# Performance work log

Measured on AMD Instinct MI355X. Metric: run time of the kernel, lower is better.

The kernel has to match this reference:

```python
import jax, jax.numpy as jnp
import numpy as np

N, H, R, E = 100000, 128, 30, 600000
EPS = 1e-5  # BatchNorm1d default eps


def _rgcn_layer(h, src, dst, etype, W, root, bias):
    """PyG RGCNConv: out = h @ root + bias + sum_r scatter_mean_r(h[src] @ W[r]).
    Mean is per (dst, relation) edge count."""
    n = h.shape[0]
    r_count = W.shape[0]
    seg = dst * r_count + etype                      # combined (dst, rel) segment id
    deg = jax.ops.segment_sum(jnp.ones_like(etype, dtype=h.dtype), seg,
                              num_segments=n * r_count)
    norm = 1.0 / jnp.maximum(deg[seg], 1.0)          # (E,) per-edge mean weight

    def body(out, inp):
        Wr, r = inp
        xr = h @ Wr                                  # (N,H) relation-transformed feats
        contrib = jnp.where((etype == r)[:, None], xr[src] * norm[:, None], 0.0)
        return out + jax.ops.segment_sum(contrib, dst, num_segments=n), None

    out0 = h @ root + bias
    out, _ = jax.lax.scan(body, out0, (W, jnp.arange(r_count)))
    return out


def _bn_relu(h, gamma, beta):
    # BatchNorm1d in training mode: biased batch statistics over the node dim
    mu = h.mean(axis=0)
    var = h.var(axis=0)
    return jax.nn.relu((h - mu) * jax.lax.rsqrt(var + EPS) * gamma + beta)


def setup_inputs() -> dict:
    key = jax.random.key(0)
    ks = jax.random.split(key, 16)
    s = 1.0 / np.sqrt(H)
    return {
        "x": jnp.arange(N, dtype=jnp.int32),
        "edge_index": jax.random.randint(ks[0], (2, E), 0, N, dtype=jnp.int32),
        "edge_type": jax.random.randint(ks[1], (E,), 0, R, dtype=jnp.int32),
        "emb": jax.random.normal(ks[2], (N, H), jnp.float32) * s,
        "W1": jax.random.normal(ks[3], (R, H, H), jnp.float32) * s,
        "root1": jax.random.normal(ks[4], (H, H), jnp.float32) * s,
        "b1": jnp.zeros((H,), jnp.float32),
        "g1": jnp.ones((H,), jnp.float32),
        "be1": jnp.zeros((H,), jnp.float32),
        "W2": jax.random.normal(ks[5], (R, H, H), jnp.float32) * s,
        "root2": jax.random.normal(ks[6], (H, H), jnp.float32) * s,
        "b2": jnp.zeros((H,), jnp.float32),
        "g2": jnp.ones((H,), jnp.float32),
        "be2": jnp.zeros((H,), jnp.float32),
    }


def reference(x, edge_index, edge_type, emb, W1, root1, b1, g1, be1,
              W2, root2, b2, g2, be2):
    src, dst = edge_index[0], edge_index[1]
    h = emb[x]                                        # (N,H) embedding lookup
    h = _bn_relu(_rgcn_layer(h, src, dst, edge_type, W1, root1, b1), g1, be1)
    h = _bn_relu(_rgcn_layer(h, src, dst, edge_type, W2, root2, b2), g2, be2)
    return h  # dropout is identity (deterministic reference)
```

## Files before the change

kernel.cpp:

```cpp
#include <hip/hip_runtime.h>
#include <hip/hip_bf16.h>

#define NN 100000
#define HH 128
#define RR 30
#define NE 600000
#define TILE 64
#define CH 64
#define EPAD (NE + RR * TILE)
#define NCHMAX (EPAD / TILE)
#define NB_PS ((NN + 255) / 256)
#define NBLK_BN 784
#define RPB_BN 128
#define BN_EPS 1e-5f

typedef __bf16 v8bf __attribute__((ext_vector_type(8)));
typedef float  v4f  __attribute__((ext_vector_type(4)));

static __device__ __forceinline__ unsigned short f2b(float f) {
    unsigned int u = __float_as_uint(f);
    unsigned int r = (u + 0x7FFF + ((u >> 16) & 1)) >> 16;
    return (unsigned short)r;
}

__global__ void k_hist(const int* __restrict__ dst, const int* __restrict__ et,
                       int* __restrict__ deg, int* __restrict__ cnt) {
    __shared__ int lh[RR];
    int t = threadIdx.x;
    if (t < RR) lh[t] = 0;
    __syncthreads();
    int i = blockIdx.x * blockDim.x + t;
    if (i < NE) {
        int d = dst[i], r = et[i];
        atomicAdd(&deg[d * RR + r], 1);
        atomicAdd(&lh[r], 1);
    }
    __syncthreads();
    if (t < RR && lh[t]) atomicAdd(&cnt[t], lh[t]);
}

__global__ void k_degsum(const int* __restrict__ deg, int* __restrict__ cnt_d) {
    int d = blockIdx.x * blockDim.x + threadIdx.x;
    if (d >= NN) return;
    int s = 0;
#pragma unroll
    for (int r = 0; r < RR; ++r) s += deg[(size_t)d * RR + r];
    cnt_d[d] = s;
}

__global__ void k_scan(const int* __restrict__ cnt, int* __restrict__ cursor,
                       int* __restrict__ totals,
                       int* __restrict__ src_s, int* __restrict__ dst_s,
                       float* __restrict__ norm_s, int* __restrict__ dpos_s,
                       int* __restrict__ chunk_rel, int need_dst) {
    __shared__ int off[RR + 1];
    if (threadIdx.x == 0) {
        int acc = 0;
        for (int r = 0; r < RR; ++r) {
            off[r] = acc;
            acc += (cnt[r] + TILE - 1) / TILE;
        }
        off[RR] = acc;
        totals[0] = acc * TILE;
    }
    __syncthreads();
    for (int r = 0; r < RR; ++r) {
        for (int c = off[r] + (int)threadIdx.x; c < off[r + 1]; c += blockDim.x)
            chunk_rel[c] = r;
        int begin = off[r] * TILE + cnt[r];
        int end   = off[r + 1] * TILE;
        for (int p = begin + (int)threadIdx.x; p < end; p += blockDim.x) {
            src_s[p] = 0; norm_s[p] = 0.f;
            dpos_s[p] = NE;
            if (need_dst) dst_s[p] = 0;
        }
    }
    if (threadIdx.x == 0)
        for (int r = 0; r < RR; ++r) cursor[r] = off[r] * TILE;
}

__global__ void k_psum1(const int* __restrict__ c, int* __restrict__ bsum) {
    __shared__ int sh[256];
    int i = blockIdx.x * 256 + threadIdx.x;
    sh[threadIdx.x] = (i < NN) ? c[i] : 0;
    __syncthreads();
    for (int s = 128; s > 0; s >>= 1) {
        if (threadIdx.x < s) sh[threadIdx.x] += sh[threadIdx.x + s];
        __syncthreads();
    }
    if (threadIdx.x == 0) bsum[blockIdx.x] = sh[0];
}

__global__ void k_psum2(int* __restrict__ bsum) {
    __shared__ int sh[512];
    int t = threadIdx.x;
    sh[t] = (t < NB_PS) ? bsum[t] : 0;
    __syncthreads();
    if (t == 0) {
        int acc = 0;
        for (int b = 0; b < NB_PS; ++b) { int v = sh[b]; sh[b] = acc; acc += v; }
    }
    __syncthreads();
    if (t < NB_PS) bsum[t] = sh[t];
}

__global__ void k_psum3(const int* __restrict__ c, const int* __restrict__ bscan,
                        int* __restrict__ off, int* __restrict__ cur) {
    __shared__ int sh[256];
    int t = threadIdx.x;
    int i = blockIdx.x * 256 + t;
    int v = (i < NN) ? c[i] : 0;
    sh[t] = v;
    __syncthreads();
    for (int s = 1; s < 256; s <<= 1) {
        int a = (t >= s) ? sh[t - s] : 0;
        __syncthreads();
        sh[t] += a;
        __syncthreads();
    }
    int excl = sh[t] - v + bscan[blockIdx.x];
    if (i < NN) { off[i] = excl; cur[i] = excl; }
    if (i == 0) off[NN] = NE;
}

__global__ void k_fillds2(const int* __restrict__ off, int* __restrict__ ds2) {
    int d = blockIdx.x * blockDim.x + threadIdx.x;
    if (d >= NN) return;
    int s = off[d], e = off[d + 1];
    for (int p = s; p < e; ++p) ds2[p] = d;
}

__global__ void k_scatter(const int* __restrict__ src, const int* __restrict__ dst,
                          const int* __restrict__ et, const int* __restrict__ deg,
                          int* __restrict__ cursor, int* __restrict__ cursor_dst,
                          int* __restrict__ src_s, int* __restrict__ dst_s,
                          float* __restrict__ norm_s, int* __restrict__ dpos_s,
                          int need_dst) {
    __shared__ int lh[RR];
    __shared__ int lbase[RR];
    int t = threadIdx.x;
    if (t < RR) lh[t] = 0;
    __syncthreads();
    int i = blockIdx.x * blockDim.x + t;
    int r = 0, d = 0, lrank = 0;
    bool valid = (i < NE);
    if (valid) {
        r = et[i]; d = dst[i];
        lrank = atomicAdd(&lh[r], 1);
    }
    __syncthreads();
    if (t < RR && lh[t]) lbase[t] = atomicAdd(&cursor[t], lh[t]);
    __syncthreads();
    if (valid) {
        int pos = lbase[r] + lrank;
        src_s[pos] = src[i];
        if (need_dst) dst_s[pos] = d;
        int dg = deg[d * RR + r];
        norm_s[pos] = 1.0f / (float)(dg > 1 ? dg : 1);
        dpos_s[pos] = atomicAdd(&cursor_dst[d], 1);
    }
}

__global__ void k_convW(const float* __restrict__ W, unsigned short* __restrict__ Wt,
                        int total) {
    int idx = blockIdx.x * blockDim.x + threadIdx.x;
    if (idx >= total) return;
    int m = idx / (HH * HH);
    int rem = idx % (HH * HH);
    int k = rem / HH, c = rem % HH;
    Wt[m * HH * HH + c * HH + k] = f2b(W[idx]);
}

__global__ void k_embed(const int* __restrict__ x, const float* __restrict__ emb,
                        unsigned short* __restrict__ hb) {
    int idx = blockIdx.x * blockDim.x + threadIdx.x;
    if (idx >= NN * HH) return;
    int i = idx / HH, j = idx % HH;
    hb[idx] = f2b(emb[x[i] * HH + j]);
}

__global__ __launch_bounds__(256) void k_rootgemm(const unsigned short* __restrict__ hb,
                                                  const unsigned short* __restrict__ rootT,
                                                  const float* __restrict__ bias,
                                                  float* __restrict__ tmp) {
    __shared__ __align__(16) unsigned short Xs[TILE][HH + 8];
    __shared__ __align__(16) unsigned short Ws[HH][HH + 8];
    int base = blockIdx.x * TILE;
    int t = threadIdx.x;

    {
        int l = t >> 2, lr = t & 3;
        int row = base + l;
        for (int i = 0; i < 4; ++i) {
            int g = lr + 4 * i;
            uint4 v = {0u, 0u, 0u, 0u};
            if (row < NN) v = *reinterpret_cast<const uint4*>(hb + (size_t)row * HH + g * 8);
            *reinterpret_cast<uint4*>(&Xs[l][g * 8]) = v;
        }
    }
    for (int i = 0; i < 8; ++i) {
        int idx = t + 256 * i;
        int row = idx >> 4, g = idx & 15;
        *reinterpret_cast<uint4*>(&Ws[row][g * 8]) =
            *reinterpret_cast<const uint4*>(rootT + row * HH + g * 8);
    }
    __syncthreads();

    int w = t >> 6, lane = t & 63;
    int lr16 = lane & 15, kg = lane >> 4;
    v4f acc[8];
    for (int n = 0; n < 8; ++n) acc[n] = (v4f){0.f, 0.f, 0.f, 0.f};
#pragma unroll
    for (int kk = 0; kk < 4; ++kk) {
        int k0 = kk * 32 + kg * 8;
        v8bf a = *reinterpret_cast<const v8bf*>(&Xs[w * 16 + lr16][k0]);
#pragma unroll
        for (int n = 0; n < 8; ++n) {
            v8bf b = *reinterpret_cast<const v8bf*>(&Ws[n * 16 + lr16][k0]);
            acc[n] = __builtin_amdgcn_mfma_f32_16x16x32_bf16(a, b, acc[n], 0, 0, 0);
        }
    }
#pragma unroll
    for (int n = 0; n < 8; ++n)
        for (int j = 0; j < 4; ++j) {
            int row = base + w * 16 + kg * 4 + j;
            int col = n * 16 + lr16;
            if (row < NN) tmp[(size_t)row * HH + col] = acc[n][j] + bias[col];
        }
}

__global__ __launch_bounds__(256) void k_edgegemm_x(const unsigned short* __restrict__ hb,
                                                    const unsigned short* __restrict__ Wt,
                                                    const int* __restrict__ src_s,
                                                    const int* __restrict__ chunk_rel,
                                                    const float* __restrict__ norm_s,
                                                    const int* __restrict__ dpos_s,
                                                    const int* __restrict__ totals,
                                                    unsigned short* __restrict__ xe) {
    int ebase = blockIdx.x * TILE;
    if (ebase >= totals[0]) return;
    __shared__ __align__(16) unsigned short Xs[TILE][HH + 8];
    __shared__ __align__(16) unsigned short Ws[HH][HH + 8];
    __shared__ int   src_l[TILE];
    __shared__ int   dpos_l[TILE];
    __shared__ float nrm_l[TILE];
    int t = threadIdx.x;
    if (t < TILE) {
        src_l[t]  = src_s[ebase + t];
        dpos_l[t] = dpos_s[ebase + t];
        nrm_l[t]  = norm_s[ebase + t];
    }
    int rel = chunk_rel[blockIdx.x];
    __syncthreads();

    {
        int l = t >> 2, lr = t & 3;
        int srow = src_l[l];
        for (int i = 0; i < 4; ++i) {
            int g = lr + 4 * i;
            *reinterpret_cast<uint4*>(&Xs[l][g * 8]) =
                *reinterpret_cast<const uint4*>(hb + (size_t)srow * HH + g * 8);
        }
    }
    const unsigned short* Wr = Wt + (size_t)rel * HH * HH;
    for (int i = 0; i < 8; ++i) {
        int idx = t + 256 * i;
        int row = idx >> 4, g = idx & 15;
        *reinterpret_cast<uint4*>(&Ws[row][g * 8]) =
            *reinterpret_cast<const uint4*>(Wr + row * HH + g * 8);
    }
    __syncthreads();

    int w = t >> 6, lane = t & 63;
    int lr16 = lane & 15, kg = lane >> 4;
    v4f acc[8];
    for (int n = 0; n < 8; ++n) acc[n] = (v4f){0.f, 0.f, 0.f, 0.f};
#pragma unroll
    for (int kk = 0; kk < 4; ++kk) {
        int k0 = kk * 32 + kg * 8;
        v8bf a = *reinterpret_cast<const v8bf*>(&Xs[w * 16 + lr16][k0]);
#pragma unroll
        for (int n = 0; n < 8; ++n) {
            v8bf b = *reinterpret_cast<const v8bf*>(&Ws[n * 16 + lr16][k0]);
            acc[n] = __builtin_amdgcn_mfma_f32_16x16x32_bf16(a, b, acc[n], 0, 0, 0);
        }
    }
    __syncthreads();
#pragma unroll
    for (int n = 0; n < 8; ++n)
        for (int j = 0; j < 4; ++j) {
            int slot = w * 16 + kg * 4 + j;
            Xs[slot][n * 16 + lr16] = f2b(acc[n][j] * nrm_l[slot]);
        }
    __syncthreads();
    {
        int l = t >> 2, lr = t & 3;
        size_t drow = (size_t)dpos_l[l];
        for (int i = 0; i < 4; ++i) {
            int g = lr + 4 * i;
            *reinterpret_cast<uint4*>(xe + drow * HH + g * 8) =
                *reinterpret_cast<uint4*>(&Xs[l][g * 8]);
        }
    }
}

__global__ __launch_bounds__(256) void k_edgegemm_at(const unsigned short* __restrict__ hb,
                                                     const unsigned short* __restrict__ Wt,
                                                     const int* __restrict__ src_s,
                                                     const int* __restrict__ dst_s,
                                                     const int* __restrict__ chunk_rel,
                                                     const float* __restrict__ norm_s,
                                                     const int* __restrict__ totals,
                                                     float* __restrict__ tmp) {
    int ebase = blockIdx.x * TILE;
    if (ebase >= totals[0]) return;
    __shared__ __align__(16) unsigned short Xs[TILE][HH + 8];
    __shared__ __align__(16) unsigned short Ws[HH][HH + 8];
    __shared__ int   src_l[TILE];
    __shared__ int   dst_l[TILE];
    __shared__ float nrm_l[TILE];
    int t = threadIdx.x;
    if (t < TILE) {
        src_l[t] = src_s[ebase + t];
        dst_l[t] = dst_s[ebase + t];
        nrm_l[t] = norm_s[ebase + t];
    }
    int rel = chunk_rel[blockIdx.x];
    __syncthreads();
    {
        int l = t >> 2, lr = t & 3;
        int srow = src_l[l];
        for (int i = 0; i < 4; ++i) {
            int g = lr + 4 * i;
            *reinterpret_cast<uint4*>(&Xs[l][g * 8]) =
                *reinterpret_cast<const uint4*>(hb + (size_t)srow * HH + g * 8);
        }
    }
    const unsigned short* Wr = Wt + (size_t)rel * HH * HH;
    for (int i = 0; i < 8; ++i) {
        int idx = t + 256 * i;
        int row = idx >> 4, g = idx & 15;
        *reinterpret_cast<uint4*>(&Ws[row][g * 8]) =
            *reinterpret_cast<const uint4*>(Wr + row * HH + g * 8);
    }
    __syncthreads();
    int w = t >> 6, lane = t & 63;
    int lr16 = lane & 15, kg = lane >> 4;
    v4f acc[8];
    for (int n = 0; n < 8; ++n) acc[n] = (v4f){0.f, 0.f, 0.f, 0.f};
#pragma unroll
    for (int kk = 0; kk < 4; ++kk) {
        int k0 = kk * 32 + kg * 8;
        v8bf a = *reinterpret_cast<const v8bf*>(&Xs[w * 16 + lr16][k0]);
#pragma unroll
        for (int n = 0; n < 8; ++n) {
            v8bf b = *reinterpret_cast<const v8bf*>(&Ws[n * 16 + lr16][k0]);
            acc[n] = __builtin_amdgcn_mfma_f32_16x16x32_bf16(a, b, acc[n], 0, 0, 0);
        }
    }
#pragma unroll
    for (int n = 0; n < 8; ++n)
        for (int j = 0; j < 4; ++j) {
            int slot = w * 16 + kg * 4 + j;
            int col  = n * 16 + lr16;
            atomicAdd(&tmp[(size_t)dst_l[slot] * HH + col], acc[n][j] * nrm_l[slot]);
        }
}

__global__ __launch_bounds__(256) void k_aggseg(const unsigned int* __restrict__ xe32,
                                                const int* __restrict__ ds2,
                                                float* __restrict__ tmp) {
    int wid = (blockIdx.x * blockDim.x + threadIdx.x) >> 6;
    int lane = threadIdx.x & 63;
    if (wid >= NE / CH) return;
    int c0 = wid * CH;

    int dme = ds2[c0 + lane];
    int dpre = __shfl_up(dme, 1);
    if (lane == 0) dpre = (c0 == 0) ? -1 : ds2[c0 - 1];
    unsigned long long bmask = __ballot(dme != dpre);
    int dnext = (c0 + CH < NE) ? ds2[c0 + CH] : -1;

    int dcur = __shfl(dme, 0);
    bool fresh = (bmask & 1ull) != 0;
    float a0 = 0.f, a1 = 0.f;
    for (int q0 = 0; q0 < CH; q0 += 16) {
        unsigned int v[16];
#pragma unroll
        for (int j = 0; j < 16; ++j)
            v[j] = xe32[(size_t)(c0 + q0 + j) * 64 + lane];
#pragma unroll
        for (int j = 0; j < 16; ++j) {
            int q = q0 + j;
            if (q && ((bmask >> q) & 1ull)) {
                float* base = tmp + (size_t)dcur * HH + lane * 2;
                if (fresh) {
                    float2* b2 = reinterpret_cast<float2*>(base);
                    float2 o = *b2; o.x += a0; o.y += a1; *b2 = o;
                } else {
                    atomicAdd(base, a0);
                    atomicAdd(base + 1, a1);
                }
                a0 = 0.f; a1 = 0.f;
                dcur = __shfl(dme, q);
                fresh = true;
            }
            a0 += __uint_as_float(v[j] << 16);
            a1 += __uint_as_float(v[j] & 0xffff0000u);
        }
    }
    {
        bool endclean = (dnext != dcur);
        float* base = tmp + (size_t)dcur * HH + lane * 2;
        if (fresh && endclean) {
            float2* b2 = reinterpret_cast<float2*>(base);
            float2 o = *b2; o.x += a0; o.y += a1; *b2 = o;
        } else {
            atomicAdd(base, a0);
            atomicAdd(base + 1, a1);
        }
    }
}

__global__ __launch_bounds__(256) void k_bnsum1(const float* __restrict__ tmp,
                                                float* __restrict__ psum,
                                                float* __restrict__ psq) {
    int t = threadIdx.x;
    int rg = t >> 5, lane = t & 31;
    int base = blockIdx.x * RPB_BN;
    v4f s = {0.f, 0.f, 0.f, 0.f}, q = {0.f, 0.f, 0.f, 0.f};
#pragma unroll 4
    for (int i = 0; i < RPB_BN / 8; ++i) {
        int row = base + rg + 8 * i;
        if (row < NN) {
            v4f v = *reinterpret_cast<const v4f*>(tmp + (size_t)row * HH + lane * 4);
            s += v; q += v * v;
        }
    }
    __shared__ v4f shs[8][32], shq[8][32];
    shs[rg][lane] = s; shq[rg][lane] = q;
    __syncthreads();
    if (rg == 0) {
        v4f ts = shs[0][lane], tq = shq[0][lane];
#pragma unroll
        for (int k = 1; k < 8; ++k) { ts += shs[k][lane]; tq += shq[k][lane]; }
        int b = blockIdx.x;
#pragma unroll
        for (int j = 0; j < 4; ++j) {
            psum[(size_t)(lane * 4 + j) * NBLK_BN + b] = ts[j];
            psq [(size_t)(lane * 4 + j) * NBLK_BN + b] = tq[j];
        }
    }
}

__global__ void k_bnsum2(const float* __restrict__ psum, const float* __restrict__ psq,
                         const float* __restrict__ g, const float* __restrict__ be,
                         float* __restrict__ sc_g, float* __restrict__ shf_g) {
    __shared__ float ssum[HH], ssq[HH];
    int t = threadIdx.x;
    int col = t & 127;
    const float* row = ((t < 128) ? psum : psq) + (size_t)col * NBLK_BN;
    v4f a = {0.f, 0.f, 0.f, 0.f};
    for (int i = 0; i < NBLK_BN / 4; ++i)
        a += *reinterpret_cast<const v4f*>(row + i * 4);
    float acc = a[0] + a[1] + a[2] + a[3];
    if (t < 128) ssum[col] = acc; else ssq[col] = acc;
    __syncthreads();
    if (t < 128) {
        float inv_n = 1.0f / (float)NN;
        float mean = ssum[col] * inv_n;
        float var = ssq[col] * inv_n - mean * mean;
        float sc = g[col] * rsqrtf(var + BN_EPS);
        sc_g[col] = sc;
        shf_g[col] = be[col] - mean * sc;
    }
}

__global__ void k_bnapply(const float* __restrict__ tmp, const float* __restrict__ sc_g,
                          const float* __restrict__ shf_g,
                          unsigned short* __restrict__ hout,
                          float* __restrict__ fout, int write_bf16) {
    int idx = blockIdx.x * blockDim.x + threadIdx.x;
    if (idx >= NN * HH / 4) return;
    int c4 = (idx & 31) * 4;
    v4f v  = *reinterpret_cast<const v4f*>(tmp + (size_t)idx * 4);
    v4f sc = *reinterpret_cast<const v4f*>(sc_g + c4);
    v4f sh = *reinterpret_cast<const v4f*>(shf_g + c4);
    v4f r;
#pragma unroll
    for (int j = 0; j < 4; ++j) r[j] = fmaxf(v[j] * sc[j] + sh[j], 0.f);
    if (write_bf16) {
        uint2 u;
        u.x = (unsigned int)f2b(r[0]) | ((unsigned int)f2b(r[1]) << 16);
        u.y = (unsigned int)f2b(r[2]) | ((unsigned int)f2b(r[3]) << 16);
        *reinterpret_cast<uint2*>(hout + (size_t)idx * 4) = u;
    } else {
        *reinterpret_cast<v4f*>(fout + (size_t)idx * 4) = r;
    }
}

constexpr size_t OFF_DEG  = 0;
constexpr size_t OFF_HB   = OFF_DEG + (size_t)NN * RR * 4;
constexpr size_t OFF_TMP  = OFF_HB + (size_t)NN * HH * 2;
constexpr size_t OFF_W1T  = OFF_TMP + (size_t)NN * HH * 4;
constexpr size_t OFF_W2T  = OFF_W1T + (size_t)RR * HH * HH * 2;
constexpr size_t OFF_R1T  = OFF_W2T + (size_t)RR * HH * HH * 2;
constexpr size_t OFF_R2T  = OFF_R1T + (size_t)HH * HH * 2;
constexpr size_t OFF_SRCS = OFF_R2T + (size_t)HH * HH * 2;
constexpr size_t OFF_DSTS = OFF_SRCS + (size_t)EPAD * 4;
constexpr size_t OFF_NRMS = OFF_DSTS + (size_t)EPAD * 4;
constexpr size_t OFF_DPOS = OFF_NRMS + (size_t)EPAD * 4;
constexpr size_t OFF_DS2  = OFF_DPOS + (size_t)EPAD * 4;
constexpr size_t OFF_CREL = OFF_DS2 + (size_t)EPAD * 4;
constexpr size_t OFF_CNTD = OFF_CREL + ((size_t)NCHMAX * 4 + 255 & ~(size_t)255);
constexpr size_t OFF_OFFD = OFF_CNTD + ((size_t)(NN + 1) * 4 + 255 & ~(size_t)255);
constexpr size_t OFF_CURD = OFF_OFFD + ((size_t)(NN + 1) * 4 + 255 & ~(size_t)255);
constexpr size_t OFF_BSUM = OFF_CURD + ((size_t)NN * 4 + 255 & ~(size_t)255);
constexpr size_t OFF_CTRL = OFF_BSUM + ((size_t)NB_PS * 4 + 255 & ~(size_t)255);
constexpr size_t OFF_SC   = OFF_CTRL + 512;
constexpr size_t OFF_SHF  = OFF_SC + 512;
constexpr size_t OFF_PSUM = OFF_SHF + 512;
constexpr size_t OFF_PSQ  = OFF_PSUM + (size_t)HH * NBLK_BN * 4;
constexpr size_t OFF_XE   = (OFF_PSQ + (size_t)HH * NBLK_BN * 4 + 255) & ~(size_t)255;
constexpr size_t WS_MIN   = OFF_XE;
constexpr size_t WS_FULL  = OFF_XE + (size_t)EPAD * HH * 2;

extern "C" void kernel_launch(void* const* d_in, const int* in_sizes, int n_in,
                              void* d_out, int out_size, void* d_ws, size_t ws_size,
                              hipStream_t stream) {
    const int*   x     = (const int*)d_in[0];
    const int*   eidx  = (const int*)d_in[1];
    const int*   et    = (const int*)d_in[2];
    const float* emb   = (const float*)d_in[3];
    const float* W1    = (const float*)d_in[4];
    const float* root1 = (const float*)d_in[5];
    const float* b1    = (const float*)d_in[6];
    const float* g1    = (const float*)d_in[7];
    const float* be1   = (const float*)d_in[8];
    const float* W2    = (const float*)d_in[9];
    const float* root2 = (const float*)d_in[10];
    const float* b2    = (const float*)d_in[11];
    const float* g2    = (const float*)d_in[12];
    const float* be2   = (const float*)d_in[13];
    float* out = (float*)d_out;

    if (ws_size < WS_MIN) return;
    const bool full = (ws_size >= WS_FULL);
    const int need_dst = full ? 0 : 1;

    char* ws = (char*)d_ws;
    int*   deg    = (int*)(ws + OFF_DEG);
    unsigned short* hb = (unsigned short*)(ws + OFF_HB);
    float* tmp    = (float*)(ws + OFF_TMP);
    unsigned short* W1t = (unsigned short*)(ws + OFF_W1T);
    unsigned short* W2t = (unsigned short*)(ws + OFF_W2T);
    unsigned short* r1t = (unsigned short*)(ws + OFF_R1T);
    unsigned short* r2t = (unsigned short*)(ws + OFF_R2T);
    int*   src_s  = (int*)(ws + OFF_SRCS);
    int*   dst_s  = (int*)(ws + OFF_DSTS);
    float* norm_s = (float*)(ws + OFF_NRMS);
    int*   dpos_s = (int*)(ws + OFF_DPOS);
    int*   ds2    = (int*)(ws + OFF_DS2);
    int*   crel   = (int*)(ws + OFF_CREL);
    int*   cnt_d  = (int*)(ws + OFF_CNTD);
    int*   off_d  = (int*)(ws + OFF_OFFD);
    int*   cur_d  = (int*)(ws + OFF_CURD);
    int*   bsum   = (int*)(ws + OFF_BSUM);
    int*   cnt    = (int*)(ws + OFF_CTRL);
    int*   cursor = cnt + 32;
    int*   totals = cnt + 64;
    float* sc_g   = (float*)(ws + OFF_SC);
    float* shf_g  = (float*)(ws + OFF_SHF);
    float* psum   = (float*)(ws + OFF_PSUM);
    float* psq    = (float*)(ws + OFF_PSQ);
    unsigned short* xe = (unsigned short*)(ws + OFF_XE);

    const int* srcp = eidx;
    const int* dstp = eidx + NE;

    hipMemsetAsync(deg, 0, (size_t)NN * RR * 4, stream);
    hipMemsetAsync(cnt, 0, 512, stream);

    k_hist<<<(NE + 255) / 256, 256, 0, stream>>>(dstp, et, deg, cnt);
    k_degsum<<<(NN + 255) / 256, 256, 0, stream>>>(deg, cnt_d);
    k_scan<<<1, 256, 0, stream>>>(cnt, cursor, totals, src_s, dst_s, norm_s,
                                  dpos_s, crel, need_dst);
    k_psum1<<<NB_PS, 256, 0, stream>>>(cnt_d, bsum);
    k_psum2<<<1, 512, 0, stream>>>(bsum);
    k_psum3<<<NB_PS, 256, 0, stream>>>(cnt_d, bsum, off_d, cur_d);
    k_fillds2<<<(NN + 255) / 256, 256, 0, stream>>>(off_d, ds2);
    k_scatter<<<(NE + 255) / 256, 256, 0, stream>>>(srcp, dstp, et, deg, cursor, cur_d,
                                                    src_s, dst_s, norm_s, dpos_s,
                                                    need_dst);
    k_convW<<<(RR * HH * HH + 255) / 256, 256, 0, stream>>>(W1, W1t, RR * HH * HH);
    k_convW<<<(RR * HH * HH + 255) / 256, 256, 0, stream>>>(W2, W2t, RR * HH * HH);
    k_convW<<<(HH * HH + 255) / 256, 256, 0, stream>>>(root1, r1t, HH * HH);
    k_convW<<<(HH * HH + 255) / 256, 256, 0, stream>>>(root2, r2t, HH * HH);
    k_embed<<<(NN * HH + 255) / 256, 256, 0, stream>>>(x, emb, hb);

    const unsigned short* Wts[2] = {W1t, W2t};
    const unsigned short* rts[2] = {r1t, r2t};
    const float* biases[2] = {b1, b2};
    const float* gs[2]     = {g1, g2};
    const float* bes[2]    = {be1, be2};

    const int nchunks = NE / CH;
    for (int layer = 0; layer < 2; ++layer) {
        k_rootgemm<<<(NN + TILE - 1) / TILE, 256, 0, stream>>>(hb, rts[layer],
                                                               biases[layer], tmp);
        if (full) {
            k_edgegemm_x<<<EPAD / TILE, 256, 0, stream>>>(hb, Wts[layer], src_s, crel,
                                                          norm_s, dpos_s, totals, xe);
            k_aggseg<<<(nchunks + 3) / 4, 256, 0, stream>>>((const unsigned int*)xe,
                                                            ds2, tmp);
        } else {
            k_edgegemm_at<<<EPAD / TILE, 256, 0, stream>>>(hb, Wts[layer], src_s, dst_s,
                                                           crel, norm_s, totals, tmp);
        }
        k_bnsum1<<<NBLK_BN, 256, 0, stream>>>(tmp, psum, psq);
        k_bnsum2<<<1, 256, 0, stream>>>(psum, psq, gs[layer], bes[layer], sc_g, shf_g);
        k_bnapply<<<(NN * HH / 4 + 255) / 256, 256, 0, stream>>>(tmp, sc_g, shf_g,
                                                                 hb, out, layer == 0);
    }
}
```

Baseline: 536.5 us.

## Load gathered rows directly into MFMA registers and store transposed results without LDS staging

The edge GEMM kernel no longer stages gathered source rows and the per-edge outputs through shared memory. Each lane now loads its source row fragments straight into registers, computes W^T·x with swapped MFMA operands so every lane holds four consecutive output columns of one edge, and writes them packed as 64-bit nontemporal stores. The segment-reduce kernel also reads the intermediate buffer with nontemporal loads. This removes LDS round trips and barriers and halves shared memory use, which may raise occupancy. In exchange the global stores become narrower (8 bytes per lane) and less coalesced than the earlier 16-byte row writes.

```diff
diff --git a/kernel.cpp b/kernel.cpp
--- a/kernel.cpp
+++ b/kernel.cpp
@@ -239,29 +239,10 @@
                                                     unsigned short* __restrict__ xe) {
     int ebase = blockIdx.x * TILE;
     if (ebase >= totals[0]) return;
-    __shared__ __align__(16) unsigned short Xs[TILE][HH + 8];
     __shared__ __align__(16) unsigned short Ws[HH][HH + 8];
-    __shared__ int   src_l[TILE];
-    __shared__ int   dpos_l[TILE];
-    __shared__ float nrm_l[TILE];
-    int t = threadIdx.x;
-    if (t < TILE) {
-        src_l[t]  = src_s[ebase + t];
-        dpos_l[t] = dpos_s[ebase + t];
-        nrm_l[t]  = norm_s[ebase + t];
-    }
+    int t = threadIdx.x;
     int rel = chunk_rel[blockIdx.x];
-    __syncthreads();
-
-    {
-        int l = t >> 2, lr = t & 3;
-        int srow = src_l[l];
-        for (int i = 0; i < 4; ++i) {
-            int g = lr + 4 * i;
-            *reinterpret_cast<uint4*>(&Xs[l][g * 8]) =
-                *reinterpret_cast<const uint4*>(hb + (size_t)srow * HH + g * 8);
-        }
-    }
+
     const unsigned short* Wr = Wt + (size_t)rel * HH * HH;
     for (int i = 0; i < 8; ++i) {
         int idx = t + 256 * i;
@@ -269,38 +250,38 @@
         *reinterpret_cast<uint4*>(&Ws[row][g * 8]) =
             *reinterpret_cast<const uint4*>(Wr + row * HH + g * 8);
     }
-    __syncthreads();
 
     int w = t >> 6, lane = t & 63;
     int lr16 = lane & 15, kg = lane >> 4;
-    v4f acc[8];
-    for (int n = 0; n < 8; ++n) acc[n] = (v4f){0.f, 0.f, 0.f, 0.f};
-#pragma unroll
-    for (int kk = 0; kk < 4; ++kk) {
-        int k0 = kk * 32 + kg * 8;
-        v8bf a = *reinterpret_cast<const v8bf*>(&Xs[w * 16 + lr16][k0]);
-#pragma unroll
-        for (int n = 0; n < 8; ++n) {
-            v8bf b = *reinterpret_cast<const v8bf*>(&Ws[n * 16 + lr16][k0]);
-            acc[n] = __builtin_amdgcn_mfma_f32_16x16x32_bf16(a, b, acc[n], 0, 0, 0);
-        }
-    }
-    __syncthreads();
-#pragma unroll
-    for (int n = 0; n < 8; ++n)
-        for (int j = 0; j < 4; ++j) {
-            int slot = w * 16 + kg * 4 + j;
-            Xs[slot][n * 16 + lr16] = f2b(acc[n][j] * nrm_l[slot]);
-        }
-    __syncthreads();
-    {
-        int l = t >> 2, lr = t & 3;
-        size_t drow = (size_t)dpos_l[l];
-        for (int i = 0; i < 4; ++i) {
-            int g = lr + 4 * i;
-            *reinterpret_cast<uint4*>(xe + drow * HH + g * 8) =
-                *reinterpret_cast<uint4*>(&Xs[l][g * 8]);
-        }
+    int slot = w * 16 + lr16;
+    int srow = src_s[ebase + slot];
+    float nrm = norm_s[ebase + slot];
+    size_t drow = (size_t)dpos_s[ebase + slot];
+
+    v8bf xf[4];
+    const unsigned short* hrow = hb + (size_t)srow * HH + kg * 8;
+#pragma unroll
+    for (int kk = 0; kk < 4; ++kk)
+        xf[kk] = *reinterpret_cast<const v8bf*>(hrow + kk * 32);
+
+    __syncthreads();
+
+    unsigned short* orow = xe + drow * HH + kg * 4;
+#pragma unroll
+    for (int n = 0; n < 8; ++n) {
+        v4f acc = {0.f, 0.f, 0.f, 0.f};
+#pragma unroll
+        for (int kk = 0; kk < 4; ++kk) {
+            v8bf wf = *reinterpret_cast<const v8bf*>(&Ws[n * 16 + lr16][kk * 32 + kg * 8]);
+            acc = __builtin_amdgcn_mfma_f32_16x16x32_bf16(wf, xf[kk], acc, 0, 0, 0);
+        }
+        unsigned long long p =
+            (unsigned long long)f2b(acc[0] * nrm)
+          | ((unsigned long long)f2b(acc[1] * nrm) << 16)
+          | ((unsigned long long)f2b(acc[2] * nrm) << 32)
+          | ((unsigned long long)f2b(acc[3] * nrm) << 48);
+        __builtin_nontemporal_store(p,
+            reinterpret_cast<unsigned long long*>(orow + n * 16));
     }
 }
 
@@ -388,7 +369,7 @@
         unsigned int v[16];
 #pragma unroll
         for (int j = 0; j < 16; ++j)
-            v[j] = xe32[(size_t)(c0 + q0 + j) * 64 + lane];
+            v[j] = __builtin_nontemporal_load(&xe32[(size_t)(c0 + q0 + j) * 64 + lane]);
 #pragma unroll
         for (int j = 0; j < 16; ++j) {
             int q = q0 + j;
```

After: 680.1 us. 26.8% more time.
